# Kernel optimization log

Measured on AMD Instinct MI355X. Metric: run time of the kernel, lower is better.

## Reference

```python
import jax, jax.numpy as jnp
import numpy as np
import math

D_MODEL = 1024
NUM_HEADS = 16
D_HEAD = D_MODEL // NUM_HEADS          # 64
N_FREQ = D_HEAD // 2 + 1               # 33 rfft bins
COMPRESSION_RATIO = 0.5


def setup_inputs() -> dict:
    key = jax.random.key(0)
    k_x, k_qkv, k_out, k_b, k_m = jax.random.split(key, 5)
    B, S = 2, 2048
    x = jax.random.normal(k_x, (B, S, D_MODEL), dtype=jnp.float32)
    # Linear weights stored as [in, out] (torch Linear uses [out, in]; math identical).
    w_qkv = jax.random.normal(k_qkv, (D_MODEL, 3 * D_MODEL), dtype=jnp.float32) / math.sqrt(D_MODEL)
    w_out = jax.random.normal(k_out, (D_MODEL, D_MODEL), dtype=jnp.float32) / math.sqrt(D_MODEL)
    b_out = jax.random.normal(k_b, (D_MODEL,), dtype=jnp.float32) * 0.01
    # Learned per-frequency-bin mask logits of AdaptiveFrequencyMask(d_state=d_head).
    # Initialized around logit(compression_ratio) with small noise.
    init_logit = math.log(COMPRESSION_RATIO / (1.0 - COMPRESSION_RATIO))
    mask_logits = init_logit + 0.1 * jax.random.normal(k_m, (N_FREQ,), dtype=jnp.float32)
    return {"x": x, "w_qkv": w_qkv, "w_out": w_out, "b_out": b_out, "mask_logits": mask_logits}


def _spectral_filter(t, mask):
    # rfft over d_head dim, apply learned soft mask, inverse rfft.  t: [B,H,S,dh]
    tf = jnp.fft.rfft(t, axis=-1)          # [B,H,S,N_FREQ] complex
    tf = tf * mask                          # broadcast real mask over bins
    return jnp.fft.irfft(tf, n=t.shape[-1], axis=-1).astype(t.dtype)


def reference(x, w_qkv, w_out, b_out, mask_logits):
    B, S, D = x.shape
    H, dh = NUM_HEADS, D_HEAD
    qkv = x @ w_qkv                                         # [B,S,3D]
    q, k, v = jnp.split(qkv, 3, axis=-1)
    # [B,S,D] -> [B,H,S,dh]
    to_heads = lambda t: t.reshape(B, S, H, dh).transpose(0, 2, 1, 3)
    q, k, v = to_heads(q), to_heads(k), to_heads(v)
    mask = jax.nn.sigmoid(mask_logits)                      # [N_FREQ]
    q = _spectral_filter(q, mask)
    k = _spectral_filter(k, mask)
    scores = jnp.einsum('bhqd,bhkd->bhqk', q, k) / math.sqrt(dh)
    attn = jax.nn.softmax(scores, axis=-1)                  # dropout p=0 (eval)
    out = jnp.einsum('bhqk,bhkd->bhqd', attn, v)
    out = out.transpose(0, 2, 1, 3).reshape(B, S, D)
    return out @ w_out + b_out
```

## Files before the change

### kernel.cpp

```cpp
#include <hip/hip_runtime.h>

#define S_LEN 2048
#define NH    16
#define DH    64
#define DM    1024
#define NQKV  3072

typedef __attribute__((ext_vector_type(8))) __bf16 bf16x8;
typedef __attribute__((ext_vector_type(4))) float  f32x4;
typedef unsigned short ushort_t;

static __device__ __forceinline__ unsigned short bf16b(float f) {
  return __builtin_bit_cast(unsigned short, (__bf16)f);
}

static __device__ __forceinline__ float exp2v(float x) {
  return __builtin_amdgcn_exp2f(x);
}

static __device__ __forceinline__ bf16x8 pack8(float4 f0, float4 f1) {
  uint4 v;
  v.x = ((unsigned)bf16b(f0.y) << 16) | bf16b(f0.x);
  v.y = ((unsigned)bf16b(f0.w) << 16) | bf16b(f0.z);
  v.z = ((unsigned)bf16b(f1.y) << 16) | bf16b(f1.x);
  v.w = ((unsigned)bf16b(f1.w) << 16) | bf16b(f1.z);
  return __builtin_bit_cast(bf16x8, v);
}

static __device__ __forceinline__ void glds16(const void* g, void* l) {
  __builtin_amdgcn_global_load_lds((const __attribute__((address_space(1))) unsigned int*)g,
                                   (__attribute__((address_space(3))) unsigned int*)l, 16, 0, 0);
}

#define OFF_WT  65536ull
#define OFF_WOT 6356992ull
#define OFF_Q   8454144ull
#define OFF_K   16842752ull
#define OFF_V   25231360ull
#define OFF_AO  33619968ull

__global__ __launch_bounds__(256) void k_prep(const float* __restrict__ wqkv,
                                              const float* __restrict__ wout,
                                              const float* __restrict__ x,
                                              const float* __restrict__ logits,
                                              unsigned short* __restrict__ Wt,
                                              unsigned short* __restrict__ Wot,
                                              unsigned short* __restrict__ xb) {
  __shared__ __align__(16) char sbuf[16640];
  int bid = blockIdx.x;
  int t = threadIdx.x;

  if (bid < 256) {
    float* msk = (float*)sbuf;
    float* Kd  = (float*)(sbuf + 144);
    ushort_t (*Fb)[72] = (ushort_t(*)[72])(sbuf + 416);
    if (t < 33) msk[t] = 1.0f / (1.0f + __expf(-logits[t]));
    __syncthreads();
    if (t < 64) {
      float acc = msk[0];
      #pragma unroll
      for (int f = 1; f < 32; ++f) {
        int r = (f * t) & 63;
        acc += 2.0f * msk[f] * __cosf((float)r * (6.28318530717958647692f / 64.0f));
      }
      acc += msk[32] * ((t & 1) ? -1.0f : 1.0f);
      Kd[t] = acc * (1.0f / 64.0f);
    }
    __syncthreads();
    for (int idx = t; idx < 4096; idx += 256) {
      int j = idx >> 6, i = idx & 63;
      Fb[j][i] = bf16b(Kd[(j - i) & 63]);
    }
    __syncthreads();

    int lane = t & 63, w = t >> 6;
    int m16 = lane & 15, quad = lane >> 4;
    int kx = bid >> 5, yy = bid & 31;
    int which = yy >> 4, h = yy & 15;
    int base = which * 1024 + h * 64;

    bf16x8 af0 = *(const bf16x8*)(&Fb[w * 16 + m16][quad * 8]);
    bf16x8 af1 = *(const bf16x8*)(&Fb[w * 16 + m16][32 + quad * 8]);

    f32x4 acc[8] = {};
    #pragma unroll 2
    for (int n = 0; n < 8; ++n) {
      const float* Wg = wqkv + (size_t)(kx * 128 + n * 16 + m16) * NQKV + base + quad * 8;
      float4 a0 = *(const float4*)(Wg);
      float4 a1 = *(const float4*)(Wg + 4);
      float4 b0 = *(const float4*)(Wg + 32);
      float4 b1 = *(const float4*)(Wg + 36);
      acc[n] = __builtin_amdgcn_mfma_f32_16x16x32_bf16(af0, pack8(a0, a1), acc[n], 0, 0, 0);
      acc[n] = __builtin_amdgcn_mfma_f32_16x16x32_bf16(af1, pack8(b0, b1), acc[n], 0, 0, 0);
    }
    float sc = (which == 0) ? 0.18033688011112042f : 1.0f;
    #pragma unroll
    for (int n = 0; n < 8; ++n) {
      #pragma unroll
      for (int r = 0; r < 4; ++r) {
        int j = w * 16 + quad * 4 + r;
        Wt[(size_t)(base + j) * DM + kx * 128 + n * 16 + m16] = bf16b(acc[n][r] * sc);
      }
    }
  } else if (bid < 768) {
    float (*Ts)[65] = (float(*)[65])sbuf;
    int b1 = bid - 256;
    if (b1 < 256) {
      int kt = b1 & 15, nt = b1 >> 4;
      int cb = 2048 + nt * 64, kbase = kt * 64;
      #pragma unroll
      for (int p = 0; p < 16; ++p) {
        int kk = p * 4 + (t >> 6);
        Ts[kk][t & 63] = wqkv[(size_t)(kbase + kk) * NQKV + cb + (t & 63)];
      }
      __syncthreads();
      #pragma unroll
      for (int p = 0; p < 16; ++p) {
        int nn = p * 4 + (t >> 6);
        Wt[(size_t)(cb + nn) * DM + kbase + (t & 63)] = bf16b(Ts[t & 63][nn]);
      }
    } else {
      int b2 = b1 - 256;
      int kt = b2 & 15, nt = b2 >> 4;
      int cb = nt * 64, kbase = kt * 64;
      #pragma unroll
      for (int p = 0; p < 16; ++p) {
        int kk = p * 4 + (t >> 6);
        Ts[kk][t & 63] = wout[(size_t)(kbase + kk) * DM + cb + (t & 63)];
      }
      __syncthreads();
      #pragma unroll
      for (int p = 0; p < 16; ++p) {
        int nn = p * 4 + (t >> 6);
        Wot[(size_t)(cb + nn) * DM + kbase + (t & 63)] = bf16b(Ts[t & 63][nn]);
      }
    }
  } else {
    size_t i = ((size_t)(bid - 768) * 256 + t) * 8;
    const float4* xp = (const float4*)(x + i);
    float4 a = xp[0], b = xp[1];
    uint4 v;
    v.x = ((unsigned)bf16b(a.y) << 16) | bf16b(a.x);
    v.y = ((unsigned)bf16b(a.w) << 16) | bf16b(a.z);
    v.z = ((unsigned)bf16b(b.y) << 16) | bf16b(b.x);
    v.w = ((unsigned)bf16b(b.w) << 16) | bf16b(b.z);
    *(uint4*)(xb + i) = v;
  }
}

template<int BM, int BN, int WCOLS, int MR, int NR>
__device__ __forceinline__ void gemm_core2(const unsigned short* __restrict__ A,
                                           const unsigned short* __restrict__ Bw,
                                           int bm, int bn, unsigned short* smem,
                                           f32x4 (&acc)[MR][NR]) {
  constexpr int SLOT = (BM + BN) * 64;
  constexpr int PA = BM / 64, PB = BN / 64;
  constexpr int L = PA + PB;
  int t = threadIdx.x, lane = t & 63, w = t >> 6;
  int m16 = lane & 15, quad = lane >> 4;
  int wr = (w / WCOLS) * (MR * 16), wc = (w % WCOLS) * (NR * 16);
  int xr = m16 & 7;
  int trow = t >> 3, tcol = t & 7;
  int gsw = (tcol ^ (trow & 7)) * 8;
  const unsigned short* Ag = A  + (size_t)(bm * BM + trow) * DM + gsw;
  const unsigned short* Bg = Bw + (size_t)(bn * BN + trow) * DM + gsw;
  unsigned short* Al = smem + trow * 64 + tcol * 8;
  unsigned short* Bl = smem + BM * 64 + trow * 64 + tcol * 8;

  #pragma unroll
  for (int s = 0; s < 2; ++s) {
    #pragma unroll
    for (int p = 0; p < PA; ++p)
      glds16(Ag + (size_t)p * 64 * DM + s * 64, Al + s * SLOT + p * 4096);
    #pragma unroll
    for (int p = 0; p < PB; ++p)
      glds16(Bg + (size_t)p * 64 * DM + s * 64, Bl + s * SLOT + p * 4096);
  }

  #pragma unroll 1
  for (int ks = 0; ks < 16; ++ks) {
    if (ks < 15) asm volatile("s_waitcnt vmcnt(%0)" :: "n"(L) : "memory");
    else         asm volatile("s_waitcnt vmcnt(0)" ::: "memory");
    __builtin_amdgcn_s_barrier();
    __builtin_amdgcn_sched_barrier(0);
    const unsigned short* As = smem + (ks & 1) * SLOT;
    const unsigned short* Bs = As + BM * 64;
    #pragma unroll
    for (int kk = 0; kk < 2; ++kk) {
      bf16x8 af[MR], bfr[NR];
      #pragma unroll
      for (int i = 0; i < MR; ++i)
        af[i] = *(const bf16x8*)(As + (wr + i * 16 + m16) * 64 + ((kk * 4 + quad) ^ xr) * 8);
      #pragma unroll
      for (int j = 0; j < NR; ++j)
        bfr[j] = *(const bf16x8*)(Bs + (wc + j * 16 + m16) * 64 + ((kk * 4 + quad) ^ xr) * 8);
      #pragma unroll
      for (int i = 0; i < MR; ++i)
        #pragma unroll
        for (int j = 0; j < NR; ++j)
          acc[i][j] = __builtin_amdgcn_mfma_f32_16x16x32_bf16(af[i], bfr[j], acc[i][j], 0, 0, 0);
    }
    if (ks < 14) {
      __builtin_amdgcn_s_barrier();
      __builtin_amdgcn_sched_barrier(0);
      int kn = ks + 2;
      #pragma unroll
      for (int p = 0; p < PA; ++p)
        glds16(Ag + (size_t)p * 64 * DM + kn * 64, Al + (ks & 1) * SLOT + p * 4096);
      #pragma unroll
      for (int p = 0; p < PB; ++p)
        glds16(Bg + (size_t)p * 64 * DM + kn * 64, Bl + (ks & 1) * SLOT + p * 4096);
    }
  }
  __syncthreads();
}

__global__ __launch_bounds__(512, 1) void k_gemm_qkv(const unsigned short* __restrict__ xb,
                                                     const unsigned short* __restrict__ Bw,
                                                     unsigned short* __restrict__ Qb,
                                                     unsigned short* __restrict__ Kb,
                                                     unsigned short* __restrict__ Vt) {
  __shared__ __align__(16) unsigned short smem[65536];
  f32x4 acc[8][4] = {};
  int bid = blockIdx.x;
  int xcd = bid & 7, loc = bid >> 3;
  int bm = xcd * 2 + (loc / 12);
  int bn = loc % 12;
  gemm_core2<256, 256, 4, 8, 4>(xb, Bw, bm, bn, smem, acc);

  int t = threadIdx.x, lane = t & 63, w = t >> 6;
  int m16 = lane & 15, quad = lane >> 4;
  int b = bm >> 3, srow = (bm & 7) * 256;
  int which = bn >> 2;
  ushort_t (*Tr)[264] = (ushort_t(*)[264])smem;

  if (which < 2) {
    unsigned short* dstB = which ? Kb : Qb;
    int hbase = (bn & 3) * 4;
    #pragma unroll
    for (int ch = 0; ch < 2; ++ch) {
      if ((w >> 2) == ch) {
        #pragma unroll
        for (int i = 0; i < 8; ++i)
          #pragma unroll
          for (int j = 0; j < 4; ++j)
            #pragma unroll
            for (int r = 0; r < 4; ++r)
              Tr[i * 16 + quad * 4 + r][(w & 3) * 64 + j * 16 + m16] = bf16b(acc[i][j][r]);
      }
      __syncthreads();
      int row = t >> 2, qh = t & 3;
      unsigned short* dst = dstB +
          ((size_t)(b * 16 + hbase + qh) * 2048 + srow + ch * 128 + row) * 64;
      #pragma unroll
      for (int p = 0; p < 8; ++p)
        *(uint4*)(dst + p * 8) = *(const uint4*)(&Tr[row][qh * 64 + p * 8]);
      __syncthreads();
    }
  } else {
    int hb = (bn - 8) * 4;
    #pragma unroll
    for (int ch = 0; ch < 2; ++ch) {
      if (((w >> 1) & 1) == ch) {
        #pragma unroll
        for (int i = 0; i < 8; ++i)
          #pragma unroll
          for (int j = 0; j < 4; ++j)
            #pragma unroll
            for (int r = 0; r < 4; ++r)
              Tr[(w & 1) * 64 + j * 16 + m16][(w >> 2) * 128 + i * 16 + quad * 4 + r] =
                  bf16b(acc[i][j][r]);
      }
      __syncthreads();
      int c = t >> 2, qh = t & 3;
      int h = hb + ch * 2 + (c >> 6), d = c & 63;
      unsigned short* dst = Vt + ((size_t)(b * 16 + h) * 64 + d) * 2048 + srow;
      #pragma unroll
      for (int p = 0; p < 8; ++p)
        *(uint4*)(dst + qh * 64 + p * 8) = *(const uint4*)(&Tr[c][qh * 64 + p * 8]);
      __syncthreads();
    }
  }
}

__global__ __launch_bounds__(512, 2) void k_attn(const unsigned short* __restrict__ Qb,
                                                 const unsigned short* __restrict__ Kb,
                                                 const unsigned short* __restrict__ Vt,
                                                 unsigned short* __restrict__ AO) {
  __shared__ __align__(16) unsigned short smem[65536];
  int t = threadIdx.x;
  int w = t >> 6, lane = t & 63;
  int m16 = lane & 15, quad = lane >> 4;
  int bid = blockIdx.x;
  int jj = bid >> 3;
  int bh = ((jj & 3) << 3) + (bid & 7);
  int qbase = (jj >> 2) * 256 + w * 32;

  const unsigned short* QpA = Qb + ((size_t)bh * S_LEN + qbase + m16) * DH + quad * 8;
  const unsigned short* QpB = QpA + 16 * DH;
  bf16x8 aq0A = *(const bf16x8*)(QpA);
  bf16x8 aq1A = *(const bf16x8*)(QpA + 32);
  bf16x8 aq0B = *(const bf16x8*)(QpB);
  bf16x8 aq1B = *(const bf16x8*)(QpB + 32);
  const unsigned short* Kbase = Kb + (size_t)bh * S_LEN * DH;
  const unsigned short* Vbase = Vt + (size_t)bh * DH * S_LEN;

  int xr = m16 & 7;
  int krow0 = ((m16 >> 2) << 3) + (m16 & 3);

  int trow = t >> 3;
  int tcol = t & 7;
  int gswzK = tcol ^ ((trow & 3) | ((trow >> 1) & 4));
  int gswzV = tcol ^ (trow & 7);
  const unsigned short* Kg = Kbase + (size_t)trow * 64 + gswzK * 8;
  const unsigned short* Vg = Vbase + (size_t)trow * S_LEN + gswzV * 8;
  unsigned short* Kl = smem + trow * 64 + tcol * 8;
  unsigned short* Vl = smem + 32768 + trow * 64 + tcol * 8;

  f32x4 oA[4] = {}, oB[4] = {};
  float lA = 0.f, lB = 0.f;
  f32x4 zero = {0.f, 0.f, 0.f, 0.f};

  #pragma unroll
  for (int tt = 0; tt < 6; ++tt) {
    glds16(Kg + (size_t)tt * 4096, Kl + tt * 4096);
    glds16(Vg + tt * 64,           Vl + tt * 4096);
  }

#define QK_TILE(KSH, SA, SB)                                                              \
    _Pragma("unroll")                                                                     \
    for (int c = 0; c < 2; ++c) {                                                         \
      _Pragma("unroll")                                                                   \
      for (int gl = 0; gl < 2; ++gl) {                                                    \
        int key = c * 32 + krow0 + gl * 4;                                                \
        bf16x8 kf0 = *(const bf16x8*)((KSH) + key * 64 + ((quad ^ xr) * 8));              \
        bf16x8 kf1 = *(const bf16x8*)((KSH) + key * 64 + (((4 + quad) ^ xr) * 8));        \
        SA[c][gl] = __builtin_amdgcn_mfma_f32_16x16x32_bf16(kf0, aq0A, zero, 0, 0, 0);    \
        SA[c][gl] = __builtin_amdgcn_mfma_f32_16x16x32_bf16(kf1, aq1A, SA[c][gl], 0, 0, 0);\
        SB[c][gl] = __builtin_amdgcn_mfma_f32_16x16x32_bf16(kf0, aq0B, zero, 0, 0, 0);    \
        SB[c][gl] = __builtin_amdgcn_mfma_f32_16x16x32_bf16(kf1, aq1B, SB[c][gl], 0, 0, 0);\
      }                                                                                   \
    }

#define SM_TILE(SA, SB, PA_, PB_)                                                         \
    _Pragma("unroll")                                                                     \
    for (int c = 0; c < 2; ++c) {                                                         \
      float a0 = exp2v(SA[c][0][0]), a1 = exp2v(SA[c][0][1]);                             \
      float a2 = exp2v(SA[c][0][2]), a3 = exp2v(SA[c][0][3]);                             \
      float a4 = exp2v(SA[c][1][0]), a5 = exp2v(SA[c][1][1]);                             \
      float a6 = exp2v(SA[c][1][2]), a7 = exp2v(SA[c][1][3]);                             \
      lA += ((a0 + a1) + (a2 + a3)) + ((a4 + a5) + (a6 + a7));                            \
      uint4 ua;                                                                           \
      ua.x = ((unsigned)bf16b(a1) << 16) | bf16b(a0);                                     \
      ua.y = ((unsigned)bf16b(a3) << 16) | bf16b(a2);                                     \
      ua.z = ((unsigned)bf16b(a5) << 16) | bf16b(a4);                                     \
      ua.w = ((unsigned)bf16b(a7) << 16) | bf16b(a6);                                     \
      PA_[c] = __builtin_bit_cast(bf16x8, ua);                                            \
      float b0 = exp2v(SB[c][0][0]), b1 = exp2v(SB[c][0][1]);                             \
      float b2 = exp2v(SB[c][0][2]), b3 = exp2v(SB[c][0][3]);                             \
      float b4 = exp2v(SB[c][1][0]), b5 = exp2v(SB[c][1][1]);                             \
      float b6 = exp2v(SB[c][1][2]), b7 = exp2v(SB[c][1][3]);                             \
      lB += ((b0 + b1) + (b2 + b3)) + ((b4 + b5) + (b6 + b7));                            \
      uint4 ub;                                                                           \
      ub.x = ((unsigned)bf16b(b1) << 16) | bf16b(b0);                                     \
      ub.y = ((unsigned)bf16b(b3) << 16) | bf16b(b2);                                     \
      ub.z = ((unsigned)bf16b(b5) << 16) | bf16b(b4);                                     \
      ub.w = ((unsigned)bf16b(b7) << 16) | bf16b(b6);                                     \
      PB_[c] = __builtin_bit_cast(bf16x8, ub);                                            \
    }

#define PV_TILE(VSH, PA_, PB_)                                                            \
    _Pragma("unroll")                                                                     \
    for (int c = 0; c < 2; ++c) {                                                         \
      _Pragma("unroll")                                                                   \
      for (int j = 0; j < 4; ++j) {                                                       \
        int dv = j * 16 + m16;                                                            \
        bf16x8 bv = *(const bf16x8*)((VSH) + dv * 64 + (((c * 4 + quad) ^ xr) * 8));      \
        oA[j] = __builtin_amdgcn_mfma_f32_16x16x32_bf16(PA_[c], bv, oA[j], 0, 0, 0);      \
        oB[j] = __builtin_amdgcn_mfma_f32_16x16x32_bf16(PB_[c], bv, oB[j], 0, 0, 0);      \
      }                                                                                   \
    }

  #pragma unroll 1
  for (int wnd = 0; wnd < 16; ++wnd) {
    if (wnd < 14)      asm volatile("s_waitcnt vmcnt(8)" ::: "memory");
    else if (wnd < 15) asm volatile("s_waitcnt vmcnt(4)" ::: "memory");
    else               asm volatile("s_waitcnt vmcnt(0)" ::: "memory");
    __builtin_amdgcn_s_barrier();
    __builtin_amdgcn_sched_barrier(0);
    if (wnd < 13) {
      int ta = 2 * wnd + 6;
      glds16(Kg + (size_t)ta * 4096,       Kl + (ta & 7) * 4096);
      glds16(Vg + ta * 64,                 Vl + (ta & 7) * 4096);
      glds16(Kg + (size_t)(ta + 1) * 4096, Kl + ((ta + 1) & 7) * 4096);
      glds16(Vg + (ta + 1) * 64,           Vl + ((ta + 1) & 7) * 4096);
    }
    int s0 = (2 * wnd) & 7, s1 = (2 * wnd + 1) & 7;
    const unsigned short* Ka  = smem + s0 * 4096;
    const unsigned short* Kbs = smem + s1 * 4096;
    const unsigned short* Va  = smem + 32768 + s0 * 4096;
    const unsigned short* Vbs = smem + 32768 + s1 * 4096;

    f32x4 sA[2][2], sB[2][2];
    __builtin_amdgcn_s_setprio(1);
    QK_TILE(Ka, sA, sB)
    __builtin_amdgcn_s_setprio(0);
    bf16x8 paA[2], paB[2];
    SM_TILE(sA, sB, paA, paB)
    f32x4 tA[2][2], tB[2][2];
    __builtin_amdgcn_s_setprio(1);
    QK_TILE(Kbs, tA, tB)
    PV_TILE(Va, paA, paB)
    __builtin_amdgcn_s_setprio(0);
    bf16x8 pbA[2], pbB[2];
    SM_TILE(tA, tB, pbA, pbB)
    __builtin_amdgcn_s_setprio(1);
    PV_TILE(Vbs, pbA, pbB)
    __builtin_amdgcn_s_setprio(0);
  }
#undef QK_TILE
#undef SM_TILE
#undef PV_TILE

  lA += __shfl_xor(lA, 16); lA += __shfl_xor(lA, 32);
  lB += __shfl_xor(lB, 16); lB += __shfl_xor(lB, 32);
  float ivA = 1.0f / lA;
  float ivB = 1.0f / lB;
  int b = bh >> 4, h = bh & 15;
  #pragma unroll
  for (int r = 0; r < 4; ++r) {
    float vA = __shfl(ivA, quad * 4 + r);
    float vB = __shfl(ivB, quad * 4 + r);
    size_t row0 = (size_t)b * S_LEN + qbase + quad * 4 + r;
    unsigned short* d0 = AO + row0 * DM + h * DH + m16;
    unsigned short* d1 = AO + (row0 + 16) * DM + h * DH + m16;
    #pragma unroll
    for (int j = 0; j < 4; ++j) {
      d0[j * 16] = bf16b(oA[j][r] * vA);
      d1[j * 16] = bf16b(oB[j][r] * vB);
    }
  }
}

__global__ __launch_bounds__(512, 1) void k_gemm_out(const unsigned short* __restrict__ A,
                                                     const unsigned short* __restrict__ Bw,
                                                     const float* __restrict__ bias,
                                                     float* __restrict__ out) {
  __shared__ __align__(16) unsigned short smem[32768];
  f32x4 acc[4][2] = {};
  int bn = blockIdx.x, bm = blockIdx.y;
  gemm_core2<128, 128, 4, 4, 2>(A, Bw, bm, bn, smem, acc);

  int t = threadIdx.x, lane = t & 63, w = t >> 6;
  int m16 = lane & 15, quad = lane >> 4;
  int wr = (w >> 2) * 64, wc = (w & 3) * 32;
  #pragma unroll
  for (int i = 0; i < 4; ++i) {
    int grow = bm * 128 + wr + i * 16 + quad * 4;
    #pragma unroll
    for (int j = 0; j < 2; ++j) {
      int gc = bn * 128 + wc + j * 16 + m16;
      float bb = bias[gc];
      #pragma unroll
      for (int r = 0; r < 4; ++r)
        out[(size_t)(grow + r) * DM + gc] = acc[i][j][r] + bb;
    }
  }
}

extern "C" void kernel_launch(void* const* d_in, const int* in_sizes, int n_in,
                              void* d_out, int out_size, void* d_ws, size_t ws_size,
                              hipStream_t stream) {
  const float* x    = (const float*)d_in[0];
  const float* wqkv = (const float*)d_in[1];
  const float* wout = (const float*)d_in[2];
  const float* bout = (const float*)d_in[3];
  const float* mlog = (const float*)d_in[4];
  char* ws = (char*)d_ws;
  unsigned short* Wt  = (unsigned short*)(ws + OFF_WT);
  unsigned short* Wot = (unsigned short*)(ws + OFF_WOT);
  unsigned short* Qb  = (unsigned short*)(ws + OFF_Q);
  unsigned short* Kb  = (unsigned short*)(ws + OFF_K);
  unsigned short* Vt  = (unsigned short*)(ws + OFF_V);
  unsigned short* xb  = (unsigned short*)(ws + OFF_AO);
  unsigned short* AO  = (unsigned short*)(ws + OFF_AO);
  float* out = (float*)d_out;

  k_prep<<<dim3(2816), dim3(256), 0, stream>>>(wqkv, wout, x, mlog, Wt, Wot, xb);
  k_gemm_qkv<<<dim3(192), dim3(512), 0, stream>>>(xb, Wt, Qb, Kb, Vt);
  k_attn<<<dim3(256), dim3(512), 0, stream>>>(Qb, Kb, Vt, AO);
  k_gemm_out<<<dim3(8, 32), dim3(512), 0, stream>>>(AO, Wot, bout, out);
}
```

Baseline: 182.8 us.

## Use 4-stage, 32-wide-K pipelined GEMM core for QKV projection

Adds a new GEMM mainloop that loads 32-element K slices into a 4-slot shared memory ring with three stages in flight, using explicit vmcnt waits and a single barrier per step. The QKV projection kernel switches to it from the previous double-buffered 64-wide-K core. The aim is to hide global-to-LDS latency behind MFMA work more deeply. In exchange, each K step does half as much MFMA work per barrier, and the new XOR swizzle pattern may cause LDS bank conflicts.

```diff
diff --git a/kernel.cpp b/kernel.cpp
--- a/kernel.cpp
+++ b/kernel.cpp
@@ -146,6 +146,75 @@
     v.w = ((unsigned)bf16b(b.w) << 16) | bf16b(b.z);
     *(uint4*)(xb + i) = v;
   }
+}
+
+template<int BM, int BN, int WCOLS, int MR, int NR>
+__device__ __forceinline__ void gemm_core3(const unsigned short* __restrict__ A,
+                                           const unsigned short* __restrict__ Bw,
+                                           int bm, int bn, unsigned short* smem,
+                                           f32x4 (&acc)[MR][NR]) {
+  constexpr int SLOT = (BM + BN) * 32;
+  constexpr int NST = DM / 32;
+  int t = threadIdx.x, lane = t & 63, w = t >> 6;
+  int m16 = lane & 15, quad = lane >> 4;
+  int wr = (w / WCOLS) * (MR * 16), wc = (w % WCOLS) * (NR * 16);
+  int qx = (quad ^ (m16 & 3)) * 8;
+
+  const unsigned short* Ag[2];
+  const unsigned short* Bg[2];
+  unsigned short* Al[2];
+  unsigned short* Bl[2];
+  #pragma unroll
+  for (int j = 0; j < 2; ++j) {
+    int ca = t + j * 512;
+    int row = ca >> 2, lc = ca & 3;
+    int sc = (lc ^ (row & 3)) * 8;
+    Ag[j] = A  + (size_t)(bm * BM + row) * DM + sc;
+    Bg[j] = Bw + (size_t)(bn * BN + row) * DM + sc;
+    Al[j] = smem + ca * 8;
+    Bl[j] = smem + BM * 32 + ca * 8;
+  }
+
+  #pragma unroll
+  for (int s = 0; s < 3; ++s) {
+    #pragma unroll
+    for (int j = 0; j < 2; ++j) {
+      glds16(Ag[j] + s * 32, Al[j] + s * SLOT);
+      glds16(Bg[j] + s * 32, Bl[j] + s * SLOT);
+    }
+  }
+
+  #pragma unroll 1
+  for (int ks = 0; ks < NST; ++ks) {
+    if (ks < NST - 2)      asm volatile("s_waitcnt vmcnt(8)" ::: "memory");
+    else if (ks < NST - 1) asm volatile("s_waitcnt vmcnt(4)" ::: "memory");
+    else                   asm volatile("s_waitcnt vmcnt(0)" ::: "memory");
+    __builtin_amdgcn_s_barrier();
+    __builtin_amdgcn_sched_barrier(0);
+    if (ks < NST - 3) {
+      int ta = ks + 3, sl = ta & 3;
+      #pragma unroll
+      for (int j = 0; j < 2; ++j) {
+        glds16(Ag[j] + ta * 32, Al[j] + sl * SLOT);
+        glds16(Bg[j] + ta * 32, Bl[j] + sl * SLOT);
+      }
+    }
+    const unsigned short* As = smem + (ks & 3) * SLOT;
+    const unsigned short* Bs = As + BM * 32;
+    bf16x8 af[MR], bfr[NR];
+    #pragma unroll
+    for (int i = 0; i < MR; ++i)
+      af[i] = *(const bf16x8*)(As + (wr + i * 16 + m16) * 32 + qx);
+    #pragma unroll
+    for (int j = 0; j < NR; ++j)
+      bfr[j] = *(const bf16x8*)(Bs + (wc + j * 16 + m16) * 32 + qx);
+    #pragma unroll
+    for (int i = 0; i < MR; ++i)
+      #pragma unroll
+      for (int j = 0; j < NR; ++j)
+        acc[i][j] = __builtin_amdgcn_mfma_f32_16x16x32_bf16(af[i], bfr[j], acc[i][j], 0, 0, 0);
+  }
+  __syncthreads();
 }
 
 template<int BM, int BN, int WCOLS, int MR, int NR>
@@ -226,7 +295,7 @@
   int xcd = bid & 7, loc = bid >> 3;
   int bm = xcd * 2 + (loc / 12);
   int bn = loc % 12;
-  gemm_core2<256, 256, 4, 8, 4>(xb, Bw, bm, bn, smem, acc);
+  gemm_core3<256, 256, 4, 8, 4>(xb, Bw, bm, bn, smem, acc);
 
   int t = threadIdx.x, lane = t & 63, w = t >> 6;
   int m16 = lane & 15, quad = lane >> 4;
```

After: 184.3 us. No clear change (+0.8%).
